# Optimization experiments

Measured on AMD Instinct MI355X. Metric: run time of the kernel, lower is better.

The kernel has to match this reference:

```python
import jax, jax.numpy as jnp
import numpy as np

HIDDEN = 1024
HEADS = 16
B, L = 2, 2048


def _xavier(key, shape):
    fan_in, fan_out = shape[1], shape[0]
    limit = float(np.sqrt(6.0 / (fan_in + fan_out)))
    return jax.random.uniform(key, shape, jnp.float32, -limit, limit)


def setup_inputs() -> dict:
    key = jax.random.key(0)
    ks = jax.random.split(key, 6)
    return {
        "query": jax.random.normal(ks[0], (B, L, HIDDEN), jnp.float32),
        "bias": jax.random.normal(ks[1], (B, 1, 1, L), jnp.float32),
        "Wq": _xavier(ks[2], (HIDDEN, HIDDEN)), "bq": jnp.zeros((HIDDEN,), jnp.float32),
        "Wk": _xavier(ks[3], (HIDDEN, HIDDEN)), "bk": jnp.zeros((HIDDEN,), jnp.float32),
        "Wv": _xavier(ks[4], (HIDDEN, HIDDEN)), "bv": jnp.zeros((HIDDEN,), jnp.float32),
        "Wo": _xavier(ks[5], (HIDDEN, HIDDEN)), "bo": jnp.zeros((HIDDEN,), jnp.float32),
    }


def _split_heads(x):
    b, l, c = x.shape
    return x.reshape(b, l, HEADS, c // HEADS).transpose(0, 2, 1, 3)  # [B,H,L,d]


def reference(query, bias, Wq, bq, Wk, bk, Wv, bv, Wo, bo):
    d_head = HIDDEN // HEADS
    q = query @ Wq.T + bq
    k = query @ Wk.T + bk
    v = query @ Wv.T + bv
    q = _split_heads(q) * (d_head ** -0.5)  # [B,H,L,d]
    k = _split_heads(k)
    v = _split_heads(v)
    logits = jnp.einsum("bhqd,bhkd->bhqk", q, k) + bias  # [B,H,L,L]
    weights = jax.nn.softmax(logits, axis=-1)
    x = jnp.einsum("bhqk,bhkd->bhqd", weights, v)  # [B,H,L,d]
    x = x.transpose(0, 2, 1, 3).reshape(query.shape[0], query.shape[1], HIDDEN)
    return x @ Wo.T + bo
```

## Files before the change

### kernel.cpp

```cpp
#include <hip/hip_runtime.h>
#include <hip/hip_fp16.h>
#include <stdint.h>

#define HIDDEN 1024
#define HEADS  16
#define DH     64
#define B_     2
#define L_     2048
#define M_TOT  (B_ * L_)
#define ELEMS  (M_TOT * HIDDEN)
#define LOG2E  1.44269504088896340736f

typedef _Float16 f16;
typedef _Float16 f16x4 __attribute__((ext_vector_type(4)));
typedef _Float16 f16x8 __attribute__((ext_vector_type(8)));
typedef float    f32x4 __attribute__((ext_vector_type(4)));
typedef uint32_t u32;
typedef __attribute__((address_space(1))) u32 gu32;
typedef __attribute__((address_space(3))) u32 su32;


__global__ __launch_bounds__(256)
void convert_f16(const float* __restrict__ query,
                 const float* __restrict__ Wq, const float* __restrict__ Wk,
                 const float* __restrict__ Wv, const float* __restrict__ Wo,
                 f16* __restrict__ Qh, f16* __restrict__ Wh)
{
    const int NQ4 = ELEMS / 4;
    const int NW4 = (HIDDEN * HIDDEN) / 4;
    const int total = NQ4 + 4 * NW4;
    for (int u = blockIdx.x * 256 + threadIdx.x; u < total; u += gridDim.x * 256) {
        float4 v; f16* dp;
        if (u < NQ4) {
            v = ((const float4*)query)[u];
            dp = Qh + (size_t)u * 4;
        } else {
            const int u2 = u - NQ4;
            const int w = u2 >> 18;
            const int off = u2 & (NW4 - 1);
            const float* W = (w == 0) ? Wq : (w == 1) ? Wk : (w == 2) ? Wv : Wo;
            v = ((const float4*)W)[off];
            dp = Wh + (size_t)u2 * 4;
        }
        f16x4 h = { (f16)v.x, (f16)v.y, (f16)v.z, (f16)v.w };
        *(f16x4*)dp = h;
    }
}

template<int TM>
__device__ __forceinline__
void gemm_loop(const f16* __restrict__ A, const f16* __restrict__ W,
               int mb, int nb, f32x4 (&acc)[TM / 32][4])
{
    __shared__ f16 As[TM * 32];
    __shared__ f16 Bs[128 * 32];

    const int tid  = threadIdx.x;
    const int lane = tid & 63;
    const int wave = tid >> 6;
    const int quad = lane >> 4;
    const int l16  = lane & 15;
    const int wm   = (wave >> 1) * (TM / 2);
    const int wn   = (wave & 1) * 64;

    constexpr int AISS = TM / 64;
    int aoff[AISS], boff[2];
#pragma unroll
    for (int q = 0; q < AISS; q++) {
        const int p16 = (wave * AISS + q) * 64 + lane;
        const int r = p16 >> 2;
        const int c8 = (p16 & 3) ^ ((r >> 1) & 3);
        aoff[q] = (mb + r) * HIDDEN + c8 * 8;
    }
#pragma unroll
    for (int q = 0; q < 2; q++) {
        const int p16 = (wave * 2 + q) * 64 + lane;
        const int r = p16 >> 2;
        const int c8 = (p16 & 3) ^ ((r >> 1) & 3);
        boff[q] = (nb + r) * HIDDEN + c8 * 8;
    }

    for (int kb = 0; kb < HIDDEN; kb += 32) {
#pragma unroll
        for (int q = 0; q < AISS; q++)
            __builtin_amdgcn_global_load_lds((gu32*)&A[aoff[q] + kb],
                                             (su32*)&As[(wave * AISS + q) * 512], 16, 0, 0);
#pragma unroll
        for (int q = 0; q < 2; q++)
            __builtin_amdgcn_global_load_lds((gu32*)&W[boff[q] + kb],
                                             (su32*)&Bs[(wave * 2 + q) * 512], 16, 0, 0);
        __syncthreads();

        f16x8 af[TM / 32], bf[4];
#pragma unroll
        for (int i = 0; i < TM / 32; i++) {
            const int r = wm + i * 16 + l16;
            af[i] = *(const f16x8*)&As[r * 32 + (quad ^ ((r >> 1) & 3)) * 8];
        }
#pragma unroll
        for (int j = 0; j < 4; j++) {
            const int r = wn + j * 16 + l16;
            bf[j] = *(const f16x8*)&Bs[r * 32 + (quad ^ ((r >> 1) & 3)) * 8];
        }
#pragma unroll
        for (int i = 0; i < TM / 32; i++)
#pragma unroll
            for (int j = 0; j < 4; j++)
                acc[i][j] = __builtin_amdgcn_mfma_f32_16x16x32_f16(af[i], bf[j], acc[i][j], 0, 0, 0);
        __syncthreads();
    }
}

__global__ __launch_bounds__(256)
void proj_qkv(const f16* __restrict__ A, const f16* __restrict__ W,
              const float* __restrict__ bq, const float* __restrict__ bk,
              const float* __restrict__ bv,
              f16* __restrict__ Qo, f16* __restrict__ Ko, f16* __restrict__ Vo)
{
    f32x4 acc[4][4] = {};
    const int mb = blockIdx.x * 128, nb = blockIdx.y * 128;
    gemm_loop<128>(A, W, mb, nb, acc);

    const int lane = threadIdx.x & 63, wave = threadIdx.x >> 6;
    const int quad = lane >> 4, l16 = lane & 15;
    const int wm = (wave >> 1) * 64, wn = (wave & 1) * 64;
    const int nsel = nb >> 10;
    const int nbase = nb & 1023;

    if (nsel < 2) {
        const float* bias = nsel ? bk : bq;
        f16* out = nsel ? Ko : Qo;
        const float scale = nsel ? 1.0f : 0.125f * LOG2E;
#pragma unroll
        for (int i = 0; i < 4; i++)
#pragma unroll
            for (int j = 0; j < 4; j++) {
                const int n1 = nbase + wn + j * 16 + l16;
                const float bn = bias[n1];
                const int h = n1 >> 6, dd = n1 & 63;
#pragma unroll
                for (int r = 0; r < 4; r++) {
                    const int m = mb + wm + i * 16 + quad * 4 + r;
                    const int b = m >> 11, l = m & (L_ - 1);
                    out[(((b * HEADS + h) * L_) + l) * DH + dd] =
                        (f16)((acc[i][j][r] + bn) * scale);
                }
            }
    } else {
#pragma unroll
        for (int i = 0; i < 4; i++)
#pragma unroll
            for (int j = 0; j < 4; j++) {
                const int n1 = nbase + wn + j * 16 + l16;
                const float bn = bv[n1];
                const int h = n1 >> 6, dd = n1 & 63;
                const int m0 = mb + wm + i * 16 + quad * 4;
                const int b = m0 >> 11, l0 = m0 & (L_ - 1);
                f16x4 pk;
#pragma unroll
                for (int r = 0; r < 4; r++) pk[r] = (f16)(acc[i][j][r] + bn);
                *(f16x4*)&Vo[((size_t)(b * HEADS + h) * DH + dd) * L_ + l0] = pk;
            }
    }
}

__global__ __launch_bounds__(256)
void proj_out(const f16* __restrict__ A, const f16* __restrict__ W,
              const float* __restrict__ bo, float* __restrict__ out)
{
    f32x4 acc[2][4] = {};
    const int mb = blockIdx.x * 64, nb = blockIdx.y * 128;
    gemm_loop<64>(A, W, mb, nb, acc);

    const int lane = threadIdx.x & 63, wave = threadIdx.x >> 6;
    const int quad = lane >> 4, l16 = lane & 15;
    const int wm = (wave >> 1) * 32, wn = (wave & 1) * 64;
#pragma unroll
    for (int i = 0; i < 2; i++)
#pragma unroll
        for (int j = 0; j < 4; j++) {
            const int n = nb + wn + j * 16 + l16;
            const float bn = bo[n];
#pragma unroll
            for (int r = 0; r < 4; r++) {
                const int m = mb + wm + i * 16 + quad * 4 + r;
                out[m * HIDDEN + n] = acc[i][j][r] + bn;
            }
        }
}

__global__ __launch_bounds__(256, 2)
void attn(const f16* __restrict__ Q, const f16* __restrict__ K,
          const f16* __restrict__ Vt, const float* __restrict__ bias,
          f16* __restrict__ X)
{
    __shared__ f16 Ks[2][64 * 64];
    __shared__ f16 Vs[2][64 * 64];
    __shared__ f16 ptile[4][2][16][68];

    const int tid  = threadIdx.x;
    const int lane = tid & 63;
    const int wave = tid >> 6;
    const int quad = lane >> 4;
    const int l16  = lane & 15;

    const int bh = blockIdx.x >> 4;
    const int b  = bh >> 4, h = bh & 15;
    const int qrow0 = (blockIdx.x & 15) * 128 + wave * 32;

    const f16* Qh  = Q  + (size_t)bh * L_ * DH;
    const f16* Kh  = K  + (size_t)bh * L_ * DH;
    const f16* Vth = Vt + (size_t)bh * DH * L_;
    const float* biasb = bias + b * L_;

    int krow[2], kcol[2];
#pragma unroll
    for (int q = 0; q < 2; q++) {
        const int grp = wave * 2 + q;
        const int r = grp * 8 + (lane >> 3);
        const int u = (lane & 7) ^ (r & 7);
        krow[q] = r; kcol[q] = u * 8;
    }

    f16x8 qf[2][2];
#pragma unroll
    for (int m = 0; m < 2; m++)
#pragma unroll
        for (int hh = 0; hh < 2; hh++)
            qf[m][hh] = *(const f16x8*)&Qh[(qrow0 + m * 16 + l16) * DH + hh * 32 + quad * 8];

#pragma unroll
    for (int q = 0; q < 2; q++) {
        __builtin_amdgcn_global_load_lds((gu32*)(Kh + (size_t)krow[q] * DH + kcol[q]),
                                         (su32*)&Ks[0][(wave * 2 + q) * 512], 16, 0, 0);
        __builtin_amdgcn_global_load_lds((gu32*)(Vth + (size_t)krow[q] * L_ + kcol[q]),
                                         (su32*)&Vs[0][(wave * 2 + q) * 512], 16, 0, 0);
    }
    float bl[4];
#pragma unroll
    for (int c = 0; c < 4; c++) bl[c] = biasb[c * 16 + l16] * LOG2E;

    f32x4 o[2][4] = {};
    float lsum[2][4] = {};
    __syncthreads();

#pragma unroll 1
    for (int kb = 0; kb < L_; kb += 64) {
        const int buf = (kb >> 6) & 1;
        const int nkb = (kb + 64 < L_) ? kb + 64 : 0;

#pragma unroll
        for (int q = 0; q < 2; q++) {
            __builtin_amdgcn_global_load_lds(
                (gu32*)(Kh + (size_t)(nkb + krow[q]) * DH + kcol[q]),
                (su32*)&Ks[buf ^ 1][(wave * 2 + q) * 512], 16, 0, 0);
            __builtin_amdgcn_global_load_lds(
                (gu32*)(Vth + (size_t)krow[q] * L_ + nkb + kcol[q]),
                (su32*)&Vs[buf ^ 1][(wave * 2 + q) * 512], 16, 0, 0);
        }
        float bln[4];
#pragma unroll
        for (int c = 0; c < 4; c++) bln[c] = biasb[nkb + c * 16 + l16] * LOG2E;

        f16x8 kf0[4], kf1[4];
#pragma unroll
        for (int c = 0; c < 4; c++) {
            const int row = c * 16 + l16;
            kf0[c] = *(const f16x8*)&Ks[buf][row * 64 + (quad ^ (row & 7)) * 8];
            kf1[c] = *(const f16x8*)&Ks[buf][row * 64 + ((quad + 4) ^ (row & 7)) * 8];
        }
        f32x4 s[2][4];
#pragma unroll
        for (int m = 0; m < 2; m++)
#pragma unroll
            for (int c = 0; c < 4; c++) {
                f32x4 z = { 0.f, 0.f, 0.f, 0.f };
                z = __builtin_amdgcn_mfma_f32_16x16x32_f16(qf[m][0], kf0[c], z, 0, 0, 0);
                s[m][c] = __builtin_amdgcn_mfma_f32_16x16x32_f16(qf[m][1], kf1[c], z, 0, 0, 0);
            }

#pragma unroll
        for (int m = 0; m < 2; m++)
#pragma unroll
            for (int c = 0; c < 4; c++)
#pragma unroll
                for (int r = 0; r < 4; r++) {
                    const float p = __builtin_amdgcn_exp2f(s[m][c][r] + bl[c]);
                    lsum[m][r] += p;
                    ptile[wave][m][quad * 4 + r][c * 16 + l16] = (f16)p;
                }

        f16x8 vf0[4], vf1[4];
#pragma unroll
        for (int t = 0; t < 4; t++) {
            const int row = t * 16 + l16;
            vf0[t] = *(const f16x8*)&Vs[buf][row * 64 + (quad ^ (row & 7)) * 8];
            vf1[t] = *(const f16x8*)&Vs[buf][row * 64 + ((quad + 4) ^ (row & 7)) * 8];
        }
        f16x8 pa[2][2];
#pragma unroll
        for (int m = 0; m < 2; m++) {
            pa[m][0] = *(const f16x8*)&ptile[wave][m][l16][quad * 8];
            pa[m][1] = *(const f16x8*)&ptile[wave][m][l16][32 + quad * 8];
        }
#pragma unroll
        for (int m = 0; m < 2; m++)
#pragma unroll
            for (int t = 0; t < 4; t++) {
                o[m][t] = __builtin_amdgcn_mfma_f32_16x16x32_f16(pa[m][0], vf0[t], o[m][t], 0, 0, 0);
                o[m][t] = __builtin_amdgcn_mfma_f32_16x16x32_f16(pa[m][1], vf1[t], o[m][t], 0, 0, 0);
            }

#pragma unroll
        for (int c = 0; c < 4; c++) bl[c] = bln[c];
        __syncthreads();
    }

#pragma unroll
    for (int x = 1; x < 16; x <<= 1)
#pragma unroll
        for (int m = 0; m < 2; m++)
#pragma unroll
            for (int r = 0; r < 4; r++)
                lsum[m][r] += __shfl_xor(lsum[m][r], x);

    float inv[2][4];
#pragma unroll
    for (int m = 0; m < 2; m++)
#pragma unroll
        for (int r = 0; r < 4; r++) inv[m][r] = 1.0f / lsum[m][r];

#pragma unroll
    for (int m = 0; m < 2; m++)
#pragma unroll
        for (int t = 0; t < 4; t++)
#pragma unroll
            for (int r = 0; r < 4; r++) {
                const int qrow = qrow0 + m * 16 + quad * 4 + r;
                X[((size_t)b * L_ + qrow) * HIDDEN + h * DH + t * 16 + l16] =
                    (f16)(o[m][t][r] * inv[m][r]);
            }
}

extern "C" void kernel_launch(void* const* d_in, const int* in_sizes, int n_in,
                              void* d_out, int out_size, void* d_ws, size_t ws_size,
                              hipStream_t stream)
{
    const float* query = (const float*)d_in[0];
    const float* bias  = (const float*)d_in[1];
    const float* Wq = (const float*)d_in[2]; const float* bq = (const float*)d_in[3];
    const float* Wk = (const float*)d_in[4]; const float* bk = (const float*)d_in[5];
    const float* Wv = (const float*)d_in[6]; const float* bv = (const float*)d_in[7];
    const float* Wo = (const float*)d_in[8]; const float* bo = (const float*)d_in[9];
    float* out = (float*)d_out;

    f16* Wh = (f16*)d_ws;
    f16* Qh = Wh + 4096 * 1024;
    f16* Kf = Qh + ELEMS;
    f16* Vf = Kf + ELEMS;
    f16* Qf = Vf + ELEMS;
    f16* Xf = Qh;

    convert_f16<<<2048, 256, 0, stream>>>(query, Wq, Wk, Wv, Wo, Qh, Wh);
    proj_qkv<<<dim3(32, 24), 256, 0, stream>>>(Qh, Wh, bq, bk, bv, Qf, Kf, Vf);
    attn<<<512, 256, 0, stream>>>(Qf, Kf, Vf, bias, Xf);
    proj_out<<<dim3(64, 8), 256, 0, stream>>>(Xf, Wh + 3072 * 1024, bo, out);
}
```

Measured before the change: 226.6 us.

## Enlarge attention query tile per wave and reshape output projection tiles

Attention now gives each wave 64 query rows instead of 32, so each block covers 256 rows and the grid is halved. K/V tiles loaded into LDS are therefore reused across twice as many queries. The QK, softmax and PV steps are interleaved per 16-row group, reusing one P tile buffer. The output projection switches to 128x64 tiles through a templated TN. The costs are more registers per thread, a dropped occupancy hint, and only 256 attention blocks, which may underfill the 256 CUs.

```diff
diff --git a/kernel.cpp b/kernel.cpp
--- a/kernel.cpp
+++ b/kernel.cpp
@@ -47,13 +47,13 @@
     }
 }
 
-template<int TM>
+template<int TM, int TN>
 __device__ __forceinline__
 void gemm_loop(const f16* __restrict__ A, const f16* __restrict__ W,
-               int mb, int nb, f32x4 (&acc)[TM / 32][4])
+               int mb, int nb, f32x4 (&acc)[TM / 32][TN / 32])
 {
     __shared__ f16 As[TM * 32];
-    __shared__ f16 Bs[128 * 32];
+    __shared__ f16 Bs[TN * 32];
 
     const int tid  = threadIdx.x;
     const int lane = tid & 63;
@@ -61,10 +61,11 @@
     const int quad = lane >> 4;
     const int l16  = lane & 15;
     const int wm   = (wave >> 1) * (TM / 2);
-    const int wn   = (wave & 1) * 64;
+    const int wn   = (wave & 1) * (TN / 2);
 
     constexpr int AISS = TM / 64;
-    int aoff[AISS], boff[2];
+    constexpr int BISS = TN / 64;
+    int aoff[AISS], boff[BISS];
 #pragma unroll
     for (int q = 0; q < AISS; q++) {
         const int p16 = (wave * AISS + q) * 64 + lane;
@@ -73,8 +74,8 @@
         aoff[q] = (mb + r) * HIDDEN + c8 * 8;
     }
 #pragma unroll
-    for (int q = 0; q < 2; q++) {
-        const int p16 = (wave * 2 + q) * 64 + lane;
+    for (int q = 0; q < BISS; q++) {
+        const int p16 = (wave * BISS + q) * 64 + lane;
         const int r = p16 >> 2;
         const int c8 = (p16 & 3) ^ ((r >> 1) & 3);
         boff[q] = (nb + r) * HIDDEN + c8 * 8;
@@ -86,26 +87,26 @@
             __builtin_amdgcn_global_load_lds((gu32*)&A[aoff[q] + kb],
                                              (su32*)&As[(wave * AISS + q) * 512], 16, 0, 0);
 #pragma unroll
-        for (int q = 0; q < 2; q++)
+        for (int q = 0; q < BISS; q++)
             __builtin_amdgcn_global_load_lds((gu32*)&W[boff[q] + kb],
-                                             (su32*)&Bs[(wave * 2 + q) * 512], 16, 0, 0);
+                                             (su32*)&Bs[(wave * BISS + q) * 512], 16, 0, 0);
         __syncthreads();
 
-        f16x8 af[TM / 32], bf[4];
+        f16x8 af[TM / 32], bf[TN / 32];
 #pragma unroll
         for (int i = 0; i < TM / 32; i++) {
             const int r = wm + i * 16 + l16;
             af[i] = *(const f16x8*)&As[r * 32 + (quad ^ ((r >> 1) & 3)) * 8];
         }
 #pragma unroll
-        for (int j = 0; j < 4; j++) {
+        for (int j = 0; j < TN / 32; j++) {
             const int r = wn + j * 16 + l16;
             bf[j] = *(const f16x8*)&Bs[r * 32 + (quad ^ ((r >> 1) & 3)) * 8];
         }
 #pragma unroll
         for (int i = 0; i < TM / 32; i++)
 #pragma unroll
-            for (int j = 0; j < 4; j++)
+            for (int j = 0; j < TN / 32; j++)
                 acc[i][j] = __builtin_amdgcn_mfma_f32_16x16x32_f16(af[i], bf[j], acc[i][j], 0, 0, 0);
         __syncthreads();
     }
@@ -119,7 +120,7 @@
 {
     f32x4 acc[4][4] = {};
     const int mb = blockIdx.x * 128, nb = blockIdx.y * 128;
-    gemm_loop<128>(A, W, mb, nb, acc);
+    gemm_loop<128, 128>(A, W, mb, nb, acc);
 
     const int lane = threadIdx.x & 63, wave = threadIdx.x >> 6;
     const int quad = lane >> 4, l16 = lane & 15;
@@ -168,17 +169,17 @@
 void proj_out(const f16* __restrict__ A, const f16* __restrict__ W,
               const float* __restrict__ bo, float* __restrict__ out)
 {
-    f32x4 acc[2][4] = {};
-    const int mb = blockIdx.x * 64, nb = blockIdx.y * 128;
-    gemm_loop<64>(A, W, mb, nb, acc);
+    f32x4 acc[4][2] = {};
+    const int mb = blockIdx.x * 128, nb = blockIdx.y * 64;
+    gemm_loop<128, 64>(A, W, mb, nb, acc);
 
     const int lane = threadIdx.x & 63, wave = threadIdx.x >> 6;
     const int quad = lane >> 4, l16 = lane & 15;
-    const int wm = (wave >> 1) * 32, wn = (wave & 1) * 64;
-#pragma unroll
-    for (int i = 0; i < 2; i++)
-#pragma unroll
-        for (int j = 0; j < 4; j++) {
+    const int wm = (wave >> 1) * 64, wn = (wave & 1) * 32;
+#pragma unroll
+    for (int i = 0; i < 4; i++)
+#pragma unroll
+        for (int j = 0; j < 2; j++) {
             const int n = nb + wn + j * 16 + l16;
             const float bn = bo[n];
 #pragma unroll
@@ -189,14 +190,14 @@
         }
 }
 
-__global__ __launch_bounds__(256, 2)
+__global__ __launch_bounds__(256)
 void attn(const f16* __restrict__ Q, const f16* __restrict__ K,
           const f16* __restrict__ Vt, const float* __restrict__ bias,
           f16* __restrict__ X)
 {
     __shared__ f16 Ks[2][64 * 64];
     __shared__ f16 Vs[2][64 * 64];
-    __shared__ f16 ptile[4][2][16][68];
+    __shared__ f16 ptile[4][16][68];
 
     const int tid  = threadIdx.x;
     const int lane = tid & 63;
@@ -204,9 +205,9 @@
     const int quad = lane >> 4;
     const int l16  = lane & 15;
 
-    const int bh = blockIdx.x >> 4;
+    const int bh = blockIdx.x >> 3;
     const int b  = bh >> 4, h = bh & 15;
-    const int qrow0 = (blockIdx.x & 15) * 128 + wave * 32;
+    const int qrow0 = (blockIdx.x & 7) * 256 + wave * 64;
 
     const f16* Qh  = Q  + (size_t)bh * L_ * DH;
     const f16* Kh  = K  + (size_t)bh * L_ * DH;
@@ -222,9 +223,9 @@
         krow[q] = r; kcol[q] = u * 8;
     }
 
-    f16x8 qf[2][2];
-#pragma unroll
-    for (int m = 0; m < 2; m++)
+    f16x8 qf[4][2];
+#pragma unroll
+    for (int m = 0; m < 4; m++)
 #pragma unroll
         for (int hh = 0; hh < 2; hh++)
             qf[m][hh] = *(const f16x8*)&Qh[(qrow0 + m * 16 + l16) * DH + hh * 32 + quad * 8];
@@ -240,8 +241,8 @@
 #pragma unroll
     for (int c = 0; c < 4; c++) bl[c] = biasb[c * 16 + l16] * LOG2E;
 
-    f32x4 o[2][4] = {};
-    float lsum[2][4] = {};
+    f32x4 o[4][4] = {};
+    float lsum[4][4] = {};
     __syncthreads();
 
 #pragma unroll 1
@@ -262,54 +263,41 @@
 #pragma unroll
         for (int c = 0; c < 4; c++) bln[c] = biasb[nkb + c * 16 + l16] * LOG2E;
 
-        f16x8 kf0[4], kf1[4];
+        f16x8 kf0[4], kf1[4], vf0[4], vf1[4];
 #pragma unroll
         for (int c = 0; c < 4; c++) {
             const int row = c * 16 + l16;
             kf0[c] = *(const f16x8*)&Ks[buf][row * 64 + (quad ^ (row & 7)) * 8];
             kf1[c] = *(const f16x8*)&Ks[buf][row * 64 + ((quad + 4) ^ (row & 7)) * 8];
-        }
-        f32x4 s[2][4];
-#pragma unroll
-        for (int m = 0; m < 2; m++)
+            vf0[c] = *(const f16x8*)&Vs[buf][row * 64 + (quad ^ (row & 7)) * 8];
+            vf1[c] = *(const f16x8*)&Vs[buf][row * 64 + ((quad + 4) ^ (row & 7)) * 8];
+        }
+
+#pragma unroll
+        for (int m = 0; m < 4; m++) {
+            f32x4 s[4];
 #pragma unroll
             for (int c = 0; c < 4; c++) {
                 f32x4 z = { 0.f, 0.f, 0.f, 0.f };
                 z = __builtin_amdgcn_mfma_f32_16x16x32_f16(qf[m][0], kf0[c], z, 0, 0, 0);
-                s[m][c] = __builtin_amdgcn_mfma_f32_16x16x32_f16(qf[m][1], kf1[c], z, 0, 0, 0);
-            }
-
-#pragma unroll
-        for (int m = 0; m < 2; m++)
+                s[c] = __builtin_amdgcn_mfma_f32_16x16x32_f16(qf[m][1], kf1[c], z, 0, 0, 0);
+            }
 #pragma unroll
             for (int c = 0; c < 4; c++)
 #pragma unroll
                 for (int r = 0; r < 4; r++) {
-                    const float p = __builtin_amdgcn_exp2f(s[m][c][r] + bl[c]);
+                    const float p = __builtin_amdgcn_exp2f(s[c][r] + bl[c]);
                     lsum[m][r] += p;
-                    ptile[wave][m][quad * 4 + r][c * 16 + l16] = (f16)p;
+                    ptile[wave][quad * 4 + r][c * 16 + l16] = (f16)p;
                 }
-
-        f16x8 vf0[4], vf1[4];
-#pragma unroll
-        for (int t = 0; t < 4; t++) {
-            const int row = t * 16 + l16;
-            vf0[t] = *(const f16x8*)&Vs[buf][row * 64 + (quad ^ (row & 7)) * 8];
-            vf1[t] = *(const f16x8*)&Vs[buf][row * 64 + ((quad + 4) ^ (row & 7)) * 8];
-        }
-        f16x8 pa[2][2];
-#pragma unroll
-        for (int m = 0; m < 2; m++) {
-            pa[m][0] = *(const f16x8*)&ptile[wave][m][l16][quad * 8];
-            pa[m][1] = *(const f16x8*)&ptile[wave][m][l16][32 + quad * 8];
-        }
-#pragma unroll
-        for (int m = 0; m < 2; m++)
+            const f16x8 pa0 = *(const f16x8*)&ptile[wave][l16][quad * 8];
+            const f16x8 pa1 = *(const f16x8*)&ptile[wave][l16][32 + quad * 8];
 #pragma unroll
             for (int t = 0; t < 4; t++) {
-                o[m][t] = __builtin_amdgcn_mfma_f32_16x16x32_f16(pa[m][0], vf0[t], o[m][t], 0, 0, 0);
-                o[m][t] = __builtin_amdgcn_mfma_f32_16x16x32_f16(pa[m][1], vf1[t], o[m][t], 0, 0, 0);
-            }
+                o[m][t] = __builtin_amdgcn_mfma_f32_16x16x32_f16(pa0, vf0[t], o[m][t], 0, 0, 0);
+                o[m][t] = __builtin_amdgcn_mfma_f32_16x16x32_f16(pa1, vf1[t], o[m][t], 0, 0, 0);
+            }
+        }
 
 #pragma unroll
         for (int c = 0; c < 4; c++) bl[c] = bln[c];
@@ -319,27 +307,25 @@
 #pragma unroll
     for (int x = 1; x < 16; x <<= 1)
 #pragma unroll
-        for (int m = 0; m < 2; m++)
+        for (int m = 0; m < 4; m++)
 #pragma unroll
             for (int r = 0; r < 4; r++)
                 lsum[m][r] += __shfl_xor(lsum[m][r], x);
 
-    float inv[2][4];
-#pragma unroll
-    for (int m = 0; m < 2; m++)
-#pragma unroll
-        for (int r = 0; r < 4; r++) inv[m][r] = 1.0f / lsum[m][r];
-
-#pragma unroll
-    for (int m = 0; m < 2; m++)
+#pragma unroll
+    for (int m = 0; m < 4; m++) {
+        float inv[4];
+#pragma unroll
+        for (int r = 0; r < 4; r++) inv[r] = 1.0f / lsum[m][r];
 #pragma unroll
         for (int t = 0; t < 4; t++)
 #pragma unroll
             for (int r = 0; r < 4; r++) {
                 const int qrow = qrow0 + m * 16 + quad * 4 + r;
                 X[((size_t)b * L_ + qrow) * HIDDEN + h * DH + t * 16 + l16] =
-                    (f16)(o[m][t][r] * inv[m][r]);
-            }
+                    (f16)(o[m][t][r] * inv[r]);
+            }
+    }
 }
 
 extern "C" void kernel_launch(void* const* d_in, const int* in_sizes, int n_in,
@@ -363,6 +349,6 @@
 
     convert_f16<<<2048, 256, 0, stream>>>(query, Wq, Wk, Wv, Wo, Qh, Wh);
     proj_qkv<<<dim3(32, 24), 256, 0, stream>>>(Qh, Wh, bq, bk, bv, Qf, Kf, Vf);
-    attn<<<512, 256, 0, stream>>>(Qf, Kf, Vf, bias, Xf);
-    proj_out<<<dim3(64, 8), 256, 0, stream>>>(Xf, Wh + 3072 * 1024, bo, out);
-}
+    attn<<<256, 256, 0, stream>>>(Qf, Kf, Vf, bias, Xf);
+    proj_out<<<dim3(32, 16), 256, 0, stream>>>(Xf, Wh + 3072 * 1024, bo, out);
+}
```

After: 246.3 us. 1.09x slower.
